# Kernel tuning notes

Measured on AMD Instinct MI355X. Metric: run time of the kernel, lower is better.

Reference implementation:

```python
import jax, jax.numpy as jnp
import numpy as np

N = 4096
D = 128
NUM_INSTANCES = 8  # samples per class in the balanced batch


def setup_inputs() -> dict:
    key = jax.random.key(0)
    x = jax.random.normal(key, (N, D), dtype=jnp.float32)
    # L2-normalize embeddings (keeps sim in [-1,1] so exp(40*sim) is finite)
    inputs = x / jnp.linalg.norm(x, axis=1, keepdims=True)
    # balanced batch: NUM_INSTANCES consecutive samples per class
    targets = (jnp.arange(N) // NUM_INSTANCES).astype(jnp.int64)
    return {"inputs": inputs, "targets": targets, "num_instances": NUM_INSTANCES}


def reference(inputs, targets, num_instances):
    n = inputs.shape[0]
    k = num_instances - 1          # positives per row (excluding self)
    sim = inputs @ inputs.T        # [n, n]

    eye = jnp.eye(n, dtype=bool)
    pos_mask = (targets[:, None] == targets[None, :]) & ~eye
    # category per entry: 0 = positive, 1 = negative, 2 = diagonal
    cat = jnp.where(pos_mask, 0, jnp.where(eye, 2, 1))
    order = jnp.argsort(cat, axis=1, stable=True)  # row-major masked_select order
    sorted_sim = jnp.take_along_axis(sim, order, axis=1)

    pos = jnp.sort(sorted_sim[:, :k], axis=1)          # [n, k]
    neg = jnpp_sort = jnp.sort(sorted_sim[:, k:n - 1], axis=1)  # [n, n-1-k]

    # GaussDistribution used .data[0] -> detached scalars (no grad through stats)
    pos_mean = jax.lax.stop_gradient(jnp.mean(pos, axis=1))
    pos_std = jax.lax.stop_gradient(jnp.sqrt(jnp.mean((pos - pos_mean[:, None]) ** 2, axis=1)))
    neg_mean = jax.lax.stop_gradient(jnp.mean(neg, axis=1))
    neg_std = jax.lax.stop_gradient(jnp.sqrt(jnp.mean((neg - neg_mean[:, None]) ** 2, axis=1)))

    inter = (neg_std * pos_mean + pos_std * neg_mean) / (pos_std + neg_std)
    inter = 0.8 * inter + 0.1                           # [n]

    pos_loss = 0.2 * jnp.mean(jnp.log1p(jnp.exp(-10.0 * (pos - inter[:, None]))), axis=1)

    # keep only negatives above (min positive - 0.05); masked mean per row
    keep = neg > (pos[:, :1] - 0.05)                    # [n, n-1-k] bool
    neg_vals = jnp.log1p(jnp.exp(40.0 * (neg - inter[:, None])))
    cnt = jnp.sum(keep, axis=1)
    neg_loss = 0.05 * jnp.sum(jnp.where(keep, neg_vals, 0.0), axis=1) / jnp.maximum(cnt, 1)

    return jnp.sum(pos_loss + neg_loss) / n
```

## Files before the change

kernel.cpp:

```cpp
#include <hip/hip_runtime.h>
#include <hip/hip_bf16.h>
#include <math.h>

namespace {

constexpr int N     = 4096;
constexpr int D     = 128;
constexpr int M     = 8;
constexpr int ROWS  = 16;
constexpr int NT    = 1024;
constexpr int NWAVE = NT / 64;
constexpr int NCH   = 16;

using short8 = __attribute__((ext_vector_type(8))) short;
using f32x4  = __attribute__((ext_vector_type(4))) float;

__device__ __forceinline__ float bf2f(unsigned short u) {
    unsigned v = (unsigned)u << 16;
    return __builtin_bit_cast(float, v);
}
__device__ __forceinline__ unsigned short f2bf(float f) {
    unsigned u = __builtin_bit_cast(unsigned, f);
    u += 0x7FFFu + ((u >> 16) & 1u);
    return (unsigned short)(u >> 16);
}
__device__ __forceinline__ float sp_fast(float z) {
    return fmaxf(z, 0.f) + __logf(1.f + __expf(-fabsf(z)));
}
__device__ __forceinline__ unsigned pack_bf(float lo, float hi) {
    __hip_bfloat162 h = __float22bfloat162_rn(make_float2(lo, hi));
    unsigned u;
    __builtin_memcpy(&u, &h, 4);
    return u;
}

__global__ void cvt_kernel(const float* __restrict__ X,
                           unsigned short* __restrict__ Xb,
                           float* __restrict__ out)
{
    const int i = blockIdx.x * blockDim.x + threadIdx.x;
    if (i == 0) out[0] = 0.f;
    const float4 v = reinterpret_cast<const float4*>(X)[i];
    ushort4 r;
    r.x = f2bf(v.x); r.y = f2bf(v.y); r.z = f2bf(v.z); r.w = f2bf(v.w);
    reinterpret_cast<ushort4*>(Xb)[i] = r;
}

__global__ __launch_bounds__(NT, 4)
void mdl_kernel(const unsigned short* __restrict__ Xb, float* __restrict__ out)
{
    __shared__ float posLds[ROWS * M];
    __shared__ float red[NWAVE * ROWS * 2];
    __shared__ float stat[ROWS * 4];

    const int t    = threadIdx.x;
    const int lane = t & 63;
    const int w    = t >> 6;
    const int lr   = lane & 15;
    const int lg   = lane >> 4;
    const int bid  = blockIdx.x;
    const int R0   = bid * ROWS;

    short8 afr0, afr1, afr2, afr3;
    {
        const unsigned short* qrow = Xb + (size_t)(R0 + lr) * D + lg * 8;
        afr0 = *reinterpret_cast<const short8*>(qrow);
        afr1 = *reinterpret_cast<const short8*>(qrow + 32);
        afr2 = *reinterpret_cast<const short8*>(qrow + 64);
        afr3 = *reinterpret_cast<const short8*>(qrow + 96);
    }

    const unsigned short* bbase = Xb + (size_t)(w * 16 + lr) * D + lg * 8;

    float sum4[4] = {0.f, 0.f, 0.f, 0.f};
    float sq4[4]  = {0.f, 0.f, 0.f, 0.f};
    unsigned pk0[NCH], pk1[NCH];

    short8 bf[2][4];
#pragma unroll
    for (int kk = 0; kk < 4; ++kk)
        bf[0][kk] = *reinterpret_cast<const short8*>(bbase + kk * 32);

#pragma unroll
    for (int cc = 0; cc < NCH; ++cc) {
        const int cur = cc & 1, nxt = cur ^ 1;
        if (cc + 1 < NCH) {
            const unsigned short* nb = bbase + (size_t)(cc + 1) * 256 * D;
#pragma unroll
            for (int kk = 0; kk < 4; ++kk)
                bf[nxt][kk] = *reinterpret_cast<const short8*>(nb + kk * 32);
        }

        f32x4 acc = {0.f, 0.f, 0.f, 0.f};
        acc = __builtin_amdgcn_mfma_f32_16x16x32_bf16(afr0, bf[cur][0], acc, 0, 0, 0);
        acc = __builtin_amdgcn_mfma_f32_16x16x32_bf16(afr1, bf[cur][1], acc, 0, 0, 0);
        acc = __builtin_amdgcn_mfma_f32_16x16x32_bf16(afr2, bf[cur][2], acc, 0, 0, 0);
        acc = __builtin_amdgcn_mfma_f32_16x16x32_bf16(afr3, bf[cur][3], acc, 0, 0, 0);

        const int chunk = cc * 16 + w;
        const bool cls  = (chunk == bid) && ((lr >> 3) == (lg >> 1));
        if (!cls) {
#pragma unroll
            for (int i = 0; i < 4; ++i) {
                const float v = acc[i];
                sum4[i] += v; sq4[i] += v * v;
            }
        } else {
#pragma unroll
            for (int i = 0; i < 4; ++i)
                posLds[(lg * 4 + i) * M + (lr & 7)] = acc[i];
        }
        pk0[cc] = pack_bf(acc[0], acc[1]);
        pk1[cc] = pack_bf(acc[2], acc[3]);
    }

#pragma unroll
    for (int i = 0; i < 4; ++i) {
        float s = sum4[i], q = sq4[i];
#pragma unroll
        for (int off = 8; off; off >>= 1) {
            s += __shfl_down(s, off, 16);
            q += __shfl_down(q, off, 16);
        }
        if (lr == 0) {
            red[(w * ROWS + lg * 4 + i) * 2]     = s;
            red[(w * ROWS + lg * 4 + i) * 2 + 1] = q;
        }
    }
    __syncthreads();

    if (t < ROWS) {
        const int r = t;
        float tot = 0.f, totsq = 0.f;
        for (int ww = 0; ww < NWAVE; ++ww) {
            tot   += red[(ww * ROWS + r) * 2];
            totsq += red[(ww * ROWS + r) * 2 + 1];
        }
        float psum = 0.f, psq = 0.f, pmin = 1e30f;
        for (int p = 0; p < M; ++p) {
            if (p == (r & 7)) continue;
            const float s = posLds[r * M + p];
            psum += s; psq += s * s; pmin = fminf(pmin, s);
        }
        const float kinv  = 1.f / (float)(M - 1);
        const float pmean = psum * kinv;
        const float pstd  = sqrtf(fmaxf(psq * kinv - pmean * pmean, 0.f));
        const float ninv  = 1.f / (float)(N - M);
        const float nmean = tot * ninv;
        const float nstd  = sqrtf(fmaxf(totsq * ninv - nmean * nmean, 0.f));
        float inter = (nstd * pmean + pstd * nmean) / (pstd + nstd);
        inter = 0.8f * inter + 0.1f;

        float pl = 0.f;
        for (int p = 0; p < M; ++p) {
            if (p == (r & 7)) continue;
            pl += sp_fast(-10.f * (posLds[r * M + p] - inter));
        }
        pl *= 0.2f * kinv;

        stat[r * 4 + 0] = inter;
        stat[r * 4 + 1] = pmin - 0.05f;
        stat[r * 4 + 2] = pl;
    }
    __syncthreads();

    float itr4[4], thr4[4];
#pragma unroll
    for (int i = 0; i < 4; ++i) {
        itr4[i] = stat[(lg * 4 + i) * 4 + 0];
        thr4[i] = stat[(lg * 4 + i) * 4 + 1];
    }
    float nls[4] = {0.f, 0.f, 0.f, 0.f};
    float cnt[4] = {0.f, 0.f, 0.f, 0.f};

#pragma unroll
    for (int cc = 0; cc < NCH; ++cc) {
        const int chunk = cc * 16 + w;
        const bool cls  = (chunk == bid) && ((lr >> 3) == (lg >> 1));
#pragma unroll
        for (int i = 0; i < 4; ++i) {
            const unsigned pkw = (i < 2) ? pk0[cc] : pk1[cc];
            const float v = bf2f((unsigned short)(pkw >> ((i & 1) * 16)));
            if (!cls && v > thr4[i]) {
                cnt[i] += 1.f;
                nls[i] += sp_fast(40.f * (v - itr4[i]));
            }
        }
    }

#pragma unroll
    for (int i = 0; i < 4; ++i) {
        float s = nls[i], c = cnt[i];
#pragma unroll
        for (int off = 8; off; off >>= 1) {
            s += __shfl_down(s, off, 16);
            c += __shfl_down(c, off, 16);
        }
        if (lr == 0) {
            red[(w * ROWS + lg * 4 + i) * 2]     = s;
            red[(w * ROWS + lg * 4 + i) * 2 + 1] = c;
        }
    }
    __syncthreads();

    if (t < ROWS) {
        float a = 0.f, b = 0.f;
        for (int ww = 0; ww < NWAVE; ++ww) {
            a += red[(ww * ROWS + t) * 2];
            b += red[(ww * ROWS + t) * 2 + 1];
        }
        stat[t * 4 + 3] = stat[t * 4 + 2] + 0.05f * a / fmaxf(b, 1.f);
    }
    __syncthreads();

    if (t == 0) {
        float acc = 0.f;
        for (int r = 0; r < ROWS; ++r) acc += stat[r * 4 + 3];
        atomicAdd(out, acc * (1.f / (float)N));
    }
}

}

extern "C" void kernel_launch(void* const* d_in, const int* in_sizes, int n_in,
                              void* d_out, int out_size, void* d_ws, size_t ws_size,
                              hipStream_t stream)
{
    const float* X = (const float*)d_in[0];
    float* out = (float*)d_out;
    unsigned short* Xb = (unsigned short*)d_ws;

    cvt_kernel<<<dim3(N * D / 4 / 256), dim3(256), 0, stream>>>(X, Xb, out);
    mdl_kernel<<<dim3(N / ROWS), dim3(NT), 0, stream>>>(Xb, out);
}
```

Baseline: 105.6 us.

## Split fused loss kernel into panel, stats and negative-loss kernels via workspace

The single fused kernel, which kept the bf16 similarity row in registers, is split into three kernels. A panel kernel computes 16-row similarity blocks over quarter column ranges and writes packed bf16 similarities plus partial sums to a 32 MB workspace. A stats kernel computes the per-row threshold statistics, and a neg kernel streams the panel to compute the masked negative loss. The aim is more parallelism and smaller blocks (256 blocks of 1024 threads become 1024 of 512), at the cost of a round trip of the full similarity matrix through memory and two extra launches.

```diff
diff --git a/kernel.cpp b/kernel.cpp
--- a/kernel.cpp
+++ b/kernel.cpp
@@ -4,13 +4,21 @@
 
 namespace {
 
-constexpr int N     = 4096;
-constexpr int D     = 128;
-constexpr int M     = 8;
-constexpr int ROWS  = 16;
-constexpr int NT    = 1024;
-constexpr int NWAVE = NT / 64;
-constexpr int NCH   = 16;
+constexpr int N    = 4096;
+constexpr int D    = 128;
+constexpr int M    = 8;
+constexpr int ROWS = 16;
+constexpr int NRS  = N / ROWS;
+constexpr int NTA  = 512;
+constexpr int NWA  = NTA / 64;
+constexpr int NQ   = 4;
+constexpr int CPW  = 8;
+
+constexpr size_t XB_OFF    = 0;
+constexpr size_t PANEL_OFF = (size_t)2 << 20;
+constexpr size_t PART_OFF  = (size_t)34 << 20;
+constexpr size_t POS_OFF   = PART_OFF + ((size_t)128 << 10);
+constexpr size_t STATS_OFF = PART_OFF + ((size_t)256 << 10);
 
 using short8 = __attribute__((ext_vector_type(8))) short;
 using f32x4  = __attribute__((ext_vector_type(4))) float;
@@ -29,9 +37,12 @@
 }
 __device__ __forceinline__ unsigned pack_bf(float lo, float hi) {
     __hip_bfloat162 h = __float22bfloat162_rn(make_float2(lo, hi));
-    unsigned u;
-    __builtin_memcpy(&u, &h, 4);
-    return u;
+    unsigned u; __builtin_memcpy(&u, &h, 4); return u;
+}
+__device__ __forceinline__ float wsum64(float v) {
+#pragma unroll
+    for (int o = 32; o; o >>= 1) v += __shfl_down(v, o, 64);
+    return v;
 }
 
 __global__ void cvt_kernel(const float* __restrict__ X,
@@ -46,59 +57,47 @@
     reinterpret_cast<ushort4*>(Xb)[i] = r;
 }
 
-__global__ __launch_bounds__(NT, 4)
-void mdl_kernel(const unsigned short* __restrict__ Xb, float* __restrict__ out)
-{
-    __shared__ float posLds[ROWS * M];
-    __shared__ float red[NWAVE * ROWS * 2];
-    __shared__ float stat[ROWS * 4];
-
+__global__ __launch_bounds__(NTA, 8)
+void panel_kernel(const unsigned short* __restrict__ Xb,
+                  unsigned* __restrict__ panelU,
+                  float* __restrict__ part, float* __restrict__ pos)
+{
+    __shared__ float red[NWA * ROWS * 2];
     const int t    = threadIdx.x;
     const int lane = t & 63;
     const int w    = t >> 6;
     const int lr   = lane & 15;
     const int lg   = lane >> 4;
-    const int bid  = blockIdx.x;
-    const int R0   = bid * ROWS;
-
-    short8 afr0, afr1, afr2, afr3;
-    {
-        const unsigned short* qrow = Xb + (size_t)(R0 + lr) * D + lg * 8;
-        afr0 = *reinterpret_cast<const short8*>(qrow);
-        afr1 = *reinterpret_cast<const short8*>(qrow + 32);
-        afr2 = *reinterpret_cast<const short8*>(qrow + 64);
-        afr3 = *reinterpret_cast<const short8*>(qrow + 96);
-    }
-
-    const unsigned short* bbase = Xb + (size_t)(w * 16 + lr) * D + lg * 8;
+    const int rs   = blockIdx.x & (NRS - 1);
+    const int q    = blockIdx.x >> 8;
+    const int R0   = rs * ROWS;
+
+    const unsigned short* qrow = Xb + (size_t)(R0 + lr) * D + lg * 8;
+    const short8 afr0 = *reinterpret_cast<const short8*>(qrow);
+    const short8 afr1 = *reinterpret_cast<const short8*>(qrow + 32);
+    const short8 afr2 = *reinterpret_cast<const short8*>(qrow + 64);
+    const short8 afr3 = *reinterpret_cast<const short8*>(qrow + 96);
 
     float sum4[4] = {0.f, 0.f, 0.f, 0.f};
     float sq4[4]  = {0.f, 0.f, 0.f, 0.f};
-    unsigned pk0[NCH], pk1[NCH];
-
-    short8 bf[2][4];
-#pragma unroll
-    for (int kk = 0; kk < 4; ++kk)
-        bf[0][kk] = *reinterpret_cast<const short8*>(bbase + kk * 32);
-
-#pragma unroll
-    for (int cc = 0; cc < NCH; ++cc) {
-        const int cur = cc & 1, nxt = cur ^ 1;
-        if (cc + 1 < NCH) {
-            const unsigned short* nb = bbase + (size_t)(cc + 1) * 256 * D;
-#pragma unroll
-            for (int kk = 0; kk < 4; ++kk)
-                bf[nxt][kk] = *reinterpret_cast<const short8*>(nb + kk * 32);
-        }
+
+#pragma unroll
+    for (int cc = 0; cc < CPW; ++cc) {
+        const int chunk = q * 64 + cc * 8 + w;
+        const int j = chunk * 16;
+        const unsigned short* brow = Xb + (size_t)(j + lr) * D + lg * 8;
+        const short8 b0 = *reinterpret_cast<const short8*>(brow);
+        const short8 b1 = *reinterpret_cast<const short8*>(brow + 32);
+        const short8 b2 = *reinterpret_cast<const short8*>(brow + 64);
+        const short8 b3 = *reinterpret_cast<const short8*>(brow + 96);
 
         f32x4 acc = {0.f, 0.f, 0.f, 0.f};
-        acc = __builtin_amdgcn_mfma_f32_16x16x32_bf16(afr0, bf[cur][0], acc, 0, 0, 0);
-        acc = __builtin_amdgcn_mfma_f32_16x16x32_bf16(afr1, bf[cur][1], acc, 0, 0, 0);
-        acc = __builtin_amdgcn_mfma_f32_16x16x32_bf16(afr2, bf[cur][2], acc, 0, 0, 0);
-        acc = __builtin_amdgcn_mfma_f32_16x16x32_bf16(afr3, bf[cur][3], acc, 0, 0, 0);
-
-        const int chunk = cc * 16 + w;
-        const bool cls  = (chunk == bid) && ((lr >> 3) == (lg >> 1));
+        acc = __builtin_amdgcn_mfma_f32_16x16x32_bf16(afr0, b0, acc, 0, 0, 0);
+        acc = __builtin_amdgcn_mfma_f32_16x16x32_bf16(afr1, b1, acc, 0, 0, 0);
+        acc = __builtin_amdgcn_mfma_f32_16x16x32_bf16(afr2, b2, acc, 0, 0, 0);
+        acc = __builtin_amdgcn_mfma_f32_16x16x32_bf16(afr3, b3, acc, 0, 0, 0);
+
+        const bool cls = (chunk == rs) && ((lr >> 3) == (lg >> 1));
         if (!cls) {
 #pragma unroll
             for (int i = 0; i < 4; ++i) {
@@ -108,115 +107,128 @@
         } else {
 #pragma unroll
             for (int i = 0; i < 4; ++i)
-                posLds[(lg * 4 + i) * M + (lr & 7)] = acc[i];
-        }
-        pk0[cc] = pack_bf(acc[0], acc[1]);
-        pk1[cc] = pack_bf(acc[2], acc[3]);
+                pos[rs * 128 + (lg * 4 + i) * 8 + (lr & 7)] = acc[i];
+        }
+        const unsigned pk0 = pack_bf(acc[0], acc[1]);
+        const unsigned pk1 = pack_bf(acc[2], acc[3]);
+        const int rp = rs * 8 + lg * 2;
+        panelU[(size_t)rp * N + j + lr]       = pk0;
+        panelU[(size_t)(rp + 1) * N + j + lr] = pk1;
     }
 
 #pragma unroll
     for (int i = 0; i < 4; ++i) {
-        float s = sum4[i], q = sq4[i];
+        float s = sum4[i], qq = sq4[i];
 #pragma unroll
         for (int off = 8; off; off >>= 1) {
-            s += __shfl_down(s, off, 16);
-            q += __shfl_down(q, off, 16);
+            s  += __shfl_down(s, off, 16);
+            qq += __shfl_down(qq, off, 16);
         }
         if (lr == 0) {
             red[(w * ROWS + lg * 4 + i) * 2]     = s;
-            red[(w * ROWS + lg * 4 + i) * 2 + 1] = q;
+            red[(w * ROWS + lg * 4 + i) * 2 + 1] = qq;
         }
     }
     __syncthreads();
-
     if (t < ROWS) {
-        const int r = t;
-        float tot = 0.f, totsq = 0.f;
-        for (int ww = 0; ww < NWAVE; ++ww) {
-            tot   += red[(ww * ROWS + r) * 2];
-            totsq += red[(ww * ROWS + r) * 2 + 1];
-        }
-        float psum = 0.f, psq = 0.f, pmin = 1e30f;
-        for (int p = 0; p < M; ++p) {
-            if (p == (r & 7)) continue;
-            const float s = posLds[r * M + p];
-            psum += s; psq += s * s; pmin = fminf(pmin, s);
-        }
-        const float kinv  = 1.f / (float)(M - 1);
-        const float pmean = psum * kinv;
-        const float pstd  = sqrtf(fmaxf(psq * kinv - pmean * pmean, 0.f));
-        const float ninv  = 1.f / (float)(N - M);
-        const float nmean = tot * ninv;
-        const float nstd  = sqrtf(fmaxf(totsq * ninv - nmean * nmean, 0.f));
-        float inter = (nstd * pmean + pstd * nmean) / (pstd + nstd);
-        inter = 0.8f * inter + 0.1f;
-
-        float pl = 0.f;
-        for (int p = 0; p < M; ++p) {
-            if (p == (r & 7)) continue;
-            pl += sp_fast(-10.f * (posLds[r * M + p] - inter));
-        }
-        pl *= 0.2f * kinv;
-
-        stat[r * 4 + 0] = inter;
-        stat[r * 4 + 1] = pmin - 0.05f;
-        stat[r * 4 + 2] = pl;
-    }
+        float s = 0.f, qq = 0.f;
+        for (int ww = 0; ww < NWA; ++ww) {
+            s  += red[(ww * ROWS + t) * 2];
+            qq += red[(ww * ROWS + t) * 2 + 1];
+        }
+        float* slot = &part[((rs * NQ + q) * ROWS + t) * 2];
+        slot[0] = s; slot[1] = qq;
+    }
+}
+
+__global__ void stats_kernel(const float* __restrict__ part,
+                             const float* __restrict__ pos,
+                             float* __restrict__ stats)
+{
+    const int r = blockIdx.x * blockDim.x + threadIdx.x;
+    const int rs = r >> 4, rl = r & 15;
+    float tot = 0.f, totsq = 0.f;
+    for (int q = 0; q < NQ; ++q) {
+        const float* slot = &part[((rs * NQ + q) * ROWS + rl) * 2];
+        tot += slot[0]; totsq += slot[1];
+    }
+    float psum = 0.f, psq = 0.f, pmin = 1e30f;
+    float pv[M];
+#pragma unroll
+    for (int p = 0; p < M; ++p) pv[p] = pos[rs * 128 + rl * 8 + p];
+#pragma unroll
+    for (int p = 0; p < M; ++p) {
+        if (p == (rl & 7)) continue;
+        psum += pv[p]; psq += pv[p] * pv[p]; pmin = fminf(pmin, pv[p]);
+    }
+    const float kinv  = 1.f / (float)(M - 1);
+    const float pmean = psum * kinv;
+    const float pstd  = sqrtf(fmaxf(psq * kinv - pmean * pmean, 0.f));
+    const float ninv  = 1.f / (float)(N - M);
+    const float nmean = tot * ninv;
+    const float nstd  = sqrtf(fmaxf(totsq * ninv - nmean * nmean, 0.f));
+    float inter = (nstd * pmean + pstd * nmean) / (pstd + nstd);
+    inter = 0.8f * inter + 0.1f;
+
+    float pl = 0.f;
+#pragma unroll
+    for (int p = 0; p < M; ++p) {
+        if (p == (rl & 7)) continue;
+        pl += sp_fast(-10.f * (pv[p] - inter));
+    }
+    pl *= 0.2f * kinv;
+
+    stats[r * 4 + 0] = inter;
+    stats[r * 4 + 1] = pmin - 0.05f;
+    stats[r * 4 + 2] = pl;
+}
+
+__global__ __launch_bounds__(256, 8)
+void neg_kernel(const unsigned* __restrict__ panelU,
+                const float* __restrict__ stats, float* __restrict__ out)
+{
+    __shared__ float red[4][4];
+    const int t  = threadIdx.x;
+    const int wv = t >> 6;
+    const int l  = t & 63;
+    const int pair = blockIdx.x;
+    const int r0 = pair * 2;
+
+    const float i0 = stats[r0 * 4 + 0], th0 = stats[r0 * 4 + 1], pl0 = stats[r0 * 4 + 2];
+    const float i1 = stats[(r0 + 1) * 4 + 0], th1 = stats[(r0 + 1) * 4 + 1],
+                pl1 = stats[(r0 + 1) * 4 + 2];
+    const int cls0 = (r0 >> 3) << 3;
+    const unsigned* base = panelU + (size_t)pair * N;
+
+    float nl0 = 0.f, c0 = 0.f, nl1 = 0.f, c1 = 0.f;
+#pragma unroll
+    for (int it = 0; it < 4; ++it) {
+        const int col0 = wv * 1024 + it * 256 + l * 4;
+        const uint4 u = *reinterpret_cast<const uint4*>(base + col0);
+#pragma unroll
+        for (int e = 0; e < 4; ++e) {
+            const int col = col0 + e;
+            if ((unsigned)(col - cls0) < 8u) continue;
+            const unsigned pw = (&u.x)[e];
+            const float vlo = bf2f((unsigned short)pw);
+            const float vhi = bf2f((unsigned short)(pw >> 16));
+            if (vlo > th0) { c0 += 1.f; nl0 += sp_fast(40.f * (vlo - i0)); }
+            if (vhi > th1) { c1 += 1.f; nl1 += sp_fast(40.f * (vhi - i1)); }
+        }
+    }
+
+    nl0 = wsum64(nl0); c0 = wsum64(c0);
+    nl1 = wsum64(nl1); c1 = wsum64(c1);
+    if (l == 0) { red[wv][0] = nl0; red[wv][1] = c0; red[wv][2] = nl1; red[wv][3] = c1; }
     __syncthreads();
-
-    float itr4[4], thr4[4];
-#pragma unroll
-    for (int i = 0; i < 4; ++i) {
-        itr4[i] = stat[(lg * 4 + i) * 4 + 0];
-        thr4[i] = stat[(lg * 4 + i) * 4 + 1];
-    }
-    float nls[4] = {0.f, 0.f, 0.f, 0.f};
-    float cnt[4] = {0.f, 0.f, 0.f, 0.f};
-
-#pragma unroll
-    for (int cc = 0; cc < NCH; ++cc) {
-        const int chunk = cc * 16 + w;
-        const bool cls  = (chunk == bid) && ((lr >> 3) == (lg >> 1));
-#pragma unroll
-        for (int i = 0; i < 4; ++i) {
-            const unsigned pkw = (i < 2) ? pk0[cc] : pk1[cc];
-            const float v = bf2f((unsigned short)(pkw >> ((i & 1) * 16)));
-            if (!cls && v > thr4[i]) {
-                cnt[i] += 1.f;
-                nls[i] += sp_fast(40.f * (v - itr4[i]));
-            }
-        }
-    }
-
-#pragma unroll
-    for (int i = 0; i < 4; ++i) {
-        float s = nls[i], c = cnt[i];
-#pragma unroll
-        for (int off = 8; off; off >>= 1) {
-            s += __shfl_down(s, off, 16);
-            c += __shfl_down(c, off, 16);
-        }
-        if (lr == 0) {
-            red[(w * ROWS + lg * 4 + i) * 2]     = s;
-            red[(w * ROWS + lg * 4 + i) * 2 + 1] = c;
-        }
-    }
-    __syncthreads();
-
-    if (t < ROWS) {
-        float a = 0.f, b = 0.f;
-        for (int ww = 0; ww < NWAVE; ++ww) {
-            a += red[(ww * ROWS + t) * 2];
-            b += red[(ww * ROWS + t) * 2 + 1];
-        }
-        stat[t * 4 + 3] = stat[t * 4 + 2] + 0.05f * a / fmaxf(b, 1.f);
-    }
-    __syncthreads();
-
     if (t == 0) {
-        float acc = 0.f;
-        for (int r = 0; r < ROWS; ++r) acc += stat[r * 4 + 3];
-        atomicAdd(out, acc * (1.f / (float)N));
+        float a0 = 0.f, b0 = 0.f, a1 = 0.f, b1 = 0.f;
+        for (int v = 0; v < 4; ++v) {
+            a0 += red[v][0]; b0 += red[v][1]; a1 += red[v][2]; b1 += red[v][3];
+        }
+        const float loss = pl0 + 0.05f * a0 / fmaxf(b0, 1.f)
+                         + pl1 + 0.05f * a1 / fmaxf(b1, 1.f);
+        atomicAdd(out, loss * (1.f / (float)N));
     }
 }
 
@@ -228,8 +240,15 @@
 {
     const float* X = (const float*)d_in[0];
     float* out = (float*)d_out;
-    unsigned short* Xb = (unsigned short*)d_ws;
+    char* ws = (char*)d_ws;
+    unsigned short* Xb = (unsigned short*)(ws + XB_OFF);
+    unsigned* panelU   = (unsigned*)(ws + PANEL_OFF);
+    float* part        = (float*)(ws + PART_OFF);
+    float* pos         = (float*)(ws + POS_OFF);
+    float* stats       = (float*)(ws + STATS_OFF);
 
     cvt_kernel<<<dim3(N * D / 4 / 256), dim3(256), 0, stream>>>(X, Xb, out);
-    mdl_kernel<<<dim3(N / ROWS), dim3(NT), 0, stream>>>(Xb, out);
-}
+    panel_kernel<<<dim3(NRS * NQ), dim3(NTA), 0, stream>>>(Xb, panelU, part, pos);
+    stats_kernel<<<dim3(N / 256), dim3(256), 0, stream>>>(part, pos, stats);
+    neg_kernel<<<dim3(N / 2), dim3(256), 0, stream>>>(panelU, stats, out);
+}
```

Measured after the change: 135.2 us. 1.28x slower.
